# Optimization experiments

Measured on AMD Instinct MI355X. Metric: run time of the kernel, lower is better.

Reference implementation:

```python
import jax, jax.numpy as jnp
import numpy as np

INPUT_DIM = 1024
OUTPUT_DIM = 1024
DEGREE = 8


def setup_inputs() -> dict:
    key = jax.random.key(0)
    k1, k2 = jax.random.split(key)
    x = jax.random.normal(k1, (8192, INPUT_DIM), dtype=jnp.float32)
    std = 1.0 / (INPUT_DIM * (DEGREE + 1))
    cheby_coeffs = jax.random.normal(k2, (INPUT_DIM, OUTPUT_DIM, DEGREE + 1), dtype=jnp.float32) * std
    return {"x": x, "cheby_coeffs": cheby_coeffs}


def reference(x, cheby_coeffs):
    # x: [B, I]; cheby_coeffs: [I, O, D+1]
    degree = cheby_coeffs.shape[-1] - 1
    t = jnp.clip(jnp.tanh(x), -0.999, 0.999)            # [B, I]
    theta = jnp.arccos(t)[..., None]                     # [B, I, 1]
    arange = jnp.arange(degree + 1, dtype=x.dtype)       # [D+1]
    basis = jnp.cos(theta * arange)                      # [B, I, D+1] Chebyshev T_d(t)
    y = jnp.einsum('bid,iod->bo', basis, cheby_coeffs)   # [B, O]
    return y
```

## Files before the change

### kernel.cpp

```cpp
#include <hip/hip_runtime.h>
#include <stdint.h>

#define B_ROWS 8192
#define I_DIM  1024
#define N_DIM  1024
#define NDEG   9
#define K_DIM  (I_DIM * (NDEG-1))

#define BM 256
#define BN 128
#define BK 64
#define NT (K_DIM / BK)

typedef __attribute__((ext_vector_type(8)))  short short8;
typedef __attribute__((ext_vector_type(16))) float f32x16;

__device__ __forceinline__ unsigned short f2bf(float f) {
  union { float f; uint32_t u; } v; v.f = f;
  uint32_t u = v.u;
  u += 0x7FFFu + ((u >> 16) & 1u);
  return (unsigned short)(u >> 16);
}

__device__ __forceinline__ float bf2f(unsigned short h) {
  union { uint32_t u; float f; } v; v.u = ((uint32_t)h) << 16;
  return v.f;
}

__device__ __forceinline__ int h2(int r) { return (r >> 2) & 7; }

__global__ __launch_bounds__(256) void prep_kernel(const float* __restrict__ x,
                                                   const float* __restrict__ cf,
                                                   unsigned short* __restrict__ A,
                                                   unsigned short* __restrict__ Bt,
                                                   float* __restrict__ bias,
                                                   int repack_blocks) {
  __shared__ unsigned short L[32][584];
  const int tid = threadIdx.x;

  if ((int)blockIdx.x < repack_blocks) {
    const int bx = blockIdx.x;
    const int i0 = (bx & 31) * 32;
    const int o0 = (bx >> 5) * 64;

    #pragma unroll
    for (int j = 0; j < 18; ++j) {
      const int f4  = j * 256 + tid;
      const int il  = f4 / 144;
      const int odq = f4 % 144;
      const float4 v = *reinterpret_cast<const float4*>(
          cf + ((size_t)(i0 + il) * N_DIM + o0) * NDEG + (size_t)odq * 4);
      ushort4 w;
      w.x = f2bf(v.x); w.y = f2bf(v.y); w.z = f2bf(v.z); w.w = f2bf(v.w);
      *reinterpret_cast<ushort4*>(&L[il][odq * 4]) = w;
    }
    __syncthreads();

    for (int od = tid; od < 576; od += 256) {
      const int o = od / 9, d = od % 9;
      if (d == 0) {
        float s = 0.f;
        #pragma unroll
        for (int il = 0; il < 32; ++il) s += bf2f(L[il][od]);
        atomicAdd(&bias[o0 + o], s);
      } else {
        const size_t base = (size_t)(o0 + o) * K_DIM + (size_t)(d - 1) * I_DIM + i0;
        #pragma unroll
        for (int ci = 0; ci < 4; ++ci) {
          uint32_t uu[4];
          #pragma unroll
          for (int p = 0; p < 4; ++p) {
            unsigned short lo = L[ci * 8 + p * 2 + 0][od];
            unsigned short hi = L[ci * 8 + p * 2 + 1][od];
            uu[p] = (uint32_t)lo | ((uint32_t)hi << 16);
          }
          uint4 u; u.x = uu[0]; u.y = uu[1]; u.z = uu[2]; u.w = uu[3];
          *reinterpret_cast<uint4*>(Bt + base + ci * 8) = u;
        }
      }
    }
  } else {
    const int b  = blockIdx.x - repack_blocks;
    const int i0 = tid * 4;
    const float4 xv = *reinterpret_cast<const float4*>(x + (size_t)b * I_DIM + i0);
    float t[4];
    t[0] = fminf(fmaxf(tanhf(xv.x), -0.999f), 0.999f);
    t[1] = fminf(fmaxf(tanhf(xv.y), -0.999f), 0.999f);
    t[2] = fminf(fmaxf(tanhf(xv.z), -0.999f), 0.999f);
    t[3] = fminf(fmaxf(tanhf(xv.w), -0.999f), 0.999f);

    unsigned short* outb = A + (size_t)b * K_DIM + i0;
    float Tp[4] = {1.f, 1.f, 1.f, 1.f};
    float Tc[4] = {t[0], t[1], t[2], t[3]};
    #pragma unroll
    for (int d = 1; d < NDEG; ++d) {
      ushort4 o4;
      o4.x = f2bf(Tc[0]); o4.y = f2bf(Tc[1]); o4.z = f2bf(Tc[2]); o4.w = f2bf(Tc[3]);
      *reinterpret_cast<ushort4*>(outb + (size_t)(d - 1) * I_DIM) = o4;
      if (d < NDEG - 1) {
        #pragma unroll
        for (int j = 0; j < 4; ++j) {
          float Tn = 2.0f * t[j] * Tc[j] - Tp[j];
          Tp[j] = Tc[j]; Tc[j] = Tn;
        }
      }
    }
  }
}

__global__ __launch_bounds__(512, 2) void gemm_kernel(const unsigned short* __restrict__ A,
                                                      const unsigned short* __restrict__ Bt,
                                                      const float* __restrict__ bias,
                                                      float* __restrict__ C) {
  extern __shared__ unsigned short sm[];
  const int tid  = threadIdx.x;
  const int lane = tid & 63;
  const int wave = tid >> 6;
  const int l31  = lane & 31;
  const int half = lane >> 5;
  const int wm   = wave >> 1;
  const int wn   = wave & 1;
  const int m0   = blockIdx.x * BM;
  const int n0   = blockIdx.y * BN;

  const int sr   = tid >> 3;
  const int slot = tid & 7;

  const unsigned short* Abase = A  + (size_t)m0 * K_DIM;
  const unsigned short* Bbase = Bt + (size_t)n0 * K_DIM;

  f32x16 acc[2][2];
  #pragma unroll
  for (int a = 0; a < 2; ++a)
    #pragma unroll
    for (int b = 0; b < 2; ++b)
      #pragma unroll
      for (int r = 0; r < 16; ++r)
        acc[a][b][r] = 0.f;

#define STAGE_A(s, bf, kk) { const int r_ = (s)*64 + sr; const int gc_ = slot ^ h2(r_);     \
    __builtin_amdgcn_global_load_lds(                                                       \
        (const __attribute__((address_space(1))) void*)(Abase + (size_t)r_*K_DIM + (kk) + gc_*8), \
        (__attribute__((address_space(3))) void*)&sm[(bf)*16384 + r_*64 + slot*8], 16, 0, 0); }
#define STAGE_B(s, bf, kk) { const int r_ = (s)*64 + sr; const int gc_ = slot ^ h2(r_);     \
    __builtin_amdgcn_global_load_lds(                                                       \
        (const __attribute__((address_space(1))) void*)(Bbase + (size_t)r_*K_DIM + (kk) + gc_*8), \
        (__attribute__((address_space(3))) void*)&sm[32768 + (bf)*8192 + r_*64 + slot*8], 16, 0, 0); }

  STAGE_A(0, 0, 0) STAGE_A(1, 0, 0) STAGE_A(2, 0, 0) STAGE_A(3, 0, 0)
  STAGE_B(0, 0, 0) STAGE_B(1, 0, 0)

  const int rowA0 = wm * 64 + l31;
  const int rowA1 = wm * 64 + 32 + l31;
  const int rowB0 = wn * 64 + l31;
  const int rowB1 = wn * 64 + 32 + l31;

  for (int kt = 0; kt < NT; ++kt) {
    const int  cur  = kt & 1;
    const int  nxt  = cur ^ 1;
    const int  k1   = (kt + 1) * BK;
    const bool more = (kt + 1 < NT);
    const unsigned short* Asc = &sm[cur * 16384];
    const unsigned short* Bsc = &sm[32768 + cur * 8192];

    if (more) { STAGE_A(0, nxt, k1) STAGE_A(1, nxt, k1) }
    if (more) asm volatile("s_waitcnt vmcnt(2)" ::: "memory");
    else      asm volatile("s_waitcnt vmcnt(0)" ::: "memory");
    __builtin_amdgcn_s_barrier();
    __builtin_amdgcn_sched_barrier(0);

    short8 av0[4], av1[4], bv0[4], bv1[4];
    #pragma unroll
    for (int ks = 0; ks < 4; ++ks) {
      const int c = ks * 2 + half;
      av0[ks] = *reinterpret_cast<const short8*>(&Asc[rowA0 * 64 + (c ^ h2(rowA0)) * 8]);
      bv0[ks] = *reinterpret_cast<const short8*>(&Bsc[rowB0 * 64 + (c ^ h2(rowB0)) * 8]);
    }
    __builtin_amdgcn_s_setprio(1);
    #pragma unroll
    for (int ks = 0; ks < 4; ++ks)
      acc[0][0] = __builtin_amdgcn_mfma_f32_32x32x16_bf16(av0[ks], bv0[ks], acc[0][0], 0, 0, 0);
    __builtin_amdgcn_s_setprio(0);
    __builtin_amdgcn_s_barrier();

    #pragma unroll
    for (int ks = 0; ks < 4; ++ks) {
      const int c = ks * 2 + half;
      bv1[ks] = *reinterpret_cast<const short8*>(&Bsc[rowB1 * 64 + (c ^ h2(rowB1)) * 8]);
    }
    if (more) { STAGE_A(2, nxt, k1) STAGE_A(3, nxt, k1) }
    __builtin_amdgcn_s_barrier();
    __builtin_amdgcn_s_setprio(1);
    #pragma unroll
    for (int ks = 0; ks < 4; ++ks)
      acc[0][1] = __builtin_amdgcn_mfma_f32_32x32x16_bf16(av0[ks], bv1[ks], acc[0][1], 0, 0, 0);
    __builtin_amdgcn_s_setprio(0);
    __builtin_amdgcn_s_barrier();

    #pragma unroll
    for (int ks = 0; ks < 4; ++ks) {
      const int c = ks * 2 + half;
      av1[ks] = *reinterpret_cast<const short8*>(&Asc[rowA1 * 64 + (c ^ h2(rowA1)) * 8]);
    }
    if (more) { STAGE_B(0, nxt, k1) STAGE_B(1, nxt, k1) }
    __builtin_amdgcn_s_barrier();
    __builtin_amdgcn_s_setprio(1);
    #pragma unroll
    for (int ks = 0; ks < 4; ++ks) {
      acc[1][0] = __builtin_amdgcn_mfma_f32_32x32x16_bf16(av1[ks], bv0[ks], acc[1][0], 0, 0, 0);
      acc[1][1] = __builtin_amdgcn_mfma_f32_32x32x16_bf16(av1[ks], bv1[ks], acc[1][1], 0, 0, 0);
    }
    __builtin_amdgcn_s_setprio(0);
    __builtin_amdgcn_s_barrier();
    __builtin_amdgcn_sched_barrier(0);
  }
#undef STAGE_A
#undef STAGE_B

  #pragma unroll
  for (int ni = 0; ni < 2; ++ni) {
    const int col  = n0 + wn * 64 + ni * 32 + l31;
    const float bc = bias[col];
    #pragma unroll
    for (int mi = 0; mi < 2; ++mi) {
      const int rbase = m0 + wm * 64 + mi * 32 + 4 * half;
      #pragma unroll
      for (int r = 0; r < 16; ++r) {
        const int row = rbase + (r & 3) + 8 * (r >> 2);
        C[(size_t)row * N_DIM + col] = acc[mi][ni][r] + bc;
      }
    }
  }
}

extern "C" void kernel_launch(void* const* d_in, const int* in_sizes, int n_in,
                              void* d_out, int out_size, void* d_ws, size_t ws_size,
                              hipStream_t stream) {
  const float* x      = (const float*)d_in[0];
  const float* coeffs = (const float*)d_in[1];
  float* y            = (float*)d_out;

  const size_t bt_bytes = (size_t)N_DIM * K_DIM * sizeof(unsigned short);
  unsigned short* Bt = (unsigned short*)d_ws;
  float* bias        = (float*)((char*)d_ws + bt_bytes);
  unsigned short* A  = (unsigned short*)((char*)d_ws + bt_bytes + 4096);

  hipMemsetAsync(bias, 0, N_DIM * sizeof(float), stream);

  hipFuncSetAttribute((const void*)gemm_kernel,
                      hipFuncAttributeMaxDynamicSharedMemorySize, 98304);

  size_t avail    = (ws_size > bt_bytes + 4096) ? (ws_size - bt_bytes - 4096) : 0;
  size_t rows_fit = avail / ((size_t)K_DIM * sizeof(unsigned short));
  int m_chunk = (int)((rows_fit / BM) * BM);
  if (m_chunk > B_ROWS) m_chunk = B_ROWS;
  if (m_chunk < BM)     m_chunk = BM;

  for (int m0 = 0; m0 < B_ROWS; m0 += m_chunk) {
    int mc = B_ROWS - m0; if (mc > m_chunk) mc = m_chunk;
    const int rb = (m0 == 0) ? 512 : 0;
    prep_kernel<<<rb + mc, 256, 0, stream>>>(x + (size_t)m0 * I_DIM, coeffs, A, Bt, bias, rb);
    gemm_kernel<<<dim3(mc / BM, N_DIM / BN), 512, 98304, stream>>>(
        A, Bt, bias, y + (size_t)m0 * N_DIM);
  }
}
```

Baseline: 274.6 us.

## Switch GEMM main loop to triple-buffered LDS with one barrier per k-tile

The main loop moves from a double-buffered LDS scheme with four barriers per k-tile and interleaved partial staging to a three-stage ring. Tile kt+2 is prefetched while tile kt is computed, and all LDS fragments are loaded up front so the 16 MFMAs run back to back. Only one waitcnt plus barrier is needed per iteration. This raises LDS use to 144 KB per block, which should still fit one 512-thread block per CU. The cost is more VGPRs held for fragments.

```diff
diff --git a/kernel.cpp b/kernel.cpp
--- a/kernel.cpp
+++ b/kernel.cpp
@@ -145,77 +145,58 @@
 #define STAGE_B(s, bf, kk) { const int r_ = (s)*64 + sr; const int gc_ = slot ^ h2(r_);     \
     __builtin_amdgcn_global_load_lds(                                                       \
         (const __attribute__((address_space(1))) void*)(Bbase + (size_t)r_*K_DIM + (kk) + gc_*8), \
-        (__attribute__((address_space(3))) void*)&sm[32768 + (bf)*8192 + r_*64 + slot*8], 16, 0, 0); }
-
-  STAGE_A(0, 0, 0) STAGE_A(1, 0, 0) STAGE_A(2, 0, 0) STAGE_A(3, 0, 0)
-  STAGE_B(0, 0, 0) STAGE_B(1, 0, 0)
+        (__attribute__((address_space(3))) void*)&sm[49152 + (bf)*8192 + r_*64 + slot*8], 16, 0, 0); }
+#define STAGE6(bf, kk) { STAGE_A(0, bf, kk) STAGE_A(1, bf, kk) STAGE_A(2, bf, kk) STAGE_A(3, bf, kk) \
+                         STAGE_B(0, bf, kk) STAGE_B(1, bf, kk) }
+
+  STAGE6(0, 0)
+  STAGE6(1, BK)
+  asm volatile("s_waitcnt vmcnt(6)" ::: "memory");
+  __builtin_amdgcn_s_barrier();
 
   const int rowA0 = wm * 64 + l31;
   const int rowA1 = wm * 64 + 32 + l31;
   const int rowB0 = wn * 64 + l31;
   const int rowB1 = wn * 64 + 32 + l31;
 
+  int cur = 0;
   for (int kt = 0; kt < NT; ++kt) {
-    const int  cur  = kt & 1;
-    const int  nxt  = cur ^ 1;
-    const int  k1   = (kt + 1) * BK;
-    const bool more = (kt + 1 < NT);
     const unsigned short* Asc = &sm[cur * 16384];
-    const unsigned short* Bsc = &sm[32768 + cur * 8192];
-
-    if (more) { STAGE_A(0, nxt, k1) STAGE_A(1, nxt, k1) }
-    if (more) asm volatile("s_waitcnt vmcnt(2)" ::: "memory");
-    else      asm volatile("s_waitcnt vmcnt(0)" ::: "memory");
-    __builtin_amdgcn_s_barrier();
-    __builtin_amdgcn_sched_barrier(0);
-
-    short8 av0[4], av1[4], bv0[4], bv1[4];
+    const unsigned short* Bsc = &sm[49152 + cur * 8192];
+    const int s2 = (cur == 0) ? 2 : cur - 1;
+
+    short8 av[2][4], bv[2][4];
     #pragma unroll
     for (int ks = 0; ks < 4; ++ks) {
       const int c = ks * 2 + half;
-      av0[ks] = *reinterpret_cast<const short8*>(&Asc[rowA0 * 64 + (c ^ h2(rowA0)) * 8]);
-      bv0[ks] = *reinterpret_cast<const short8*>(&Bsc[rowB0 * 64 + (c ^ h2(rowB0)) * 8]);
-    }
+      av[0][ks] = *reinterpret_cast<const short8*>(&Asc[rowA0 * 64 + (c ^ h2(rowA0)) * 8]);
+      av[1][ks] = *reinterpret_cast<const short8*>(&Asc[rowA1 * 64 + (c ^ h2(rowA1)) * 8]);
+      bv[0][ks] = *reinterpret_cast<const short8*>(&Bsc[rowB0 * 64 + (c ^ h2(rowB0)) * 8]);
+      bv[1][ks] = *reinterpret_cast<const short8*>(&Bsc[rowB1 * 64 + (c ^ h2(rowB1)) * 8]);
+    }
+
+    if (kt + 2 < NT) { STAGE6(s2, (kt + 2) * BK) }
+
     __builtin_amdgcn_s_setprio(1);
     #pragma unroll
-    for (int ks = 0; ks < 4; ++ks)
-      acc[0][0] = __builtin_amdgcn_mfma_f32_32x32x16_bf16(av0[ks], bv0[ks], acc[0][0], 0, 0, 0);
+    for (int ks = 0; ks < 4; ++ks) {
+      acc[0][0] = __builtin_amdgcn_mfma_f32_32x32x16_bf16(av[0][ks], bv[0][ks], acc[0][0], 0, 0, 0);
+      acc[0][1] = __builtin_amdgcn_mfma_f32_32x32x16_bf16(av[0][ks], bv[1][ks], acc[0][1], 0, 0, 0);
+      acc[1][0] = __builtin_amdgcn_mfma_f32_32x32x16_bf16(av[1][ks], bv[0][ks], acc[1][0], 0, 0, 0);
+      acc[1][1] = __builtin_amdgcn_mfma_f32_32x32x16_bf16(av[1][ks], bv[1][ks], acc[1][1], 0, 0, 0);
+    }
     __builtin_amdgcn_s_setprio(0);
-    __builtin_amdgcn_s_barrier();
-
-    #pragma unroll
-    for (int ks = 0; ks < 4; ++ks) {
-      const int c = ks * 2 + half;
-      bv1[ks] = *reinterpret_cast<const short8*>(&Bsc[rowB1 * 64 + (c ^ h2(rowB1)) * 8]);
-    }
-    if (more) { STAGE_A(2, nxt, k1) STAGE_A(3, nxt, k1) }
-    __builtin_amdgcn_s_barrier();
-    __builtin_amdgcn_s_setprio(1);
-    #pragma unroll
-    for (int ks = 0; ks < 4; ++ks)
-      acc[0][1] = __builtin_amdgcn_mfma_f32_32x32x16_bf16(av0[ks], bv1[ks], acc[0][1], 0, 0, 0);
-    __builtin_amdgcn_s_setprio(0);
-    __builtin_amdgcn_s_barrier();
-
-    #pragma unroll
-    for (int ks = 0; ks < 4; ++ks) {
-      const int c = ks * 2 + half;
-      av1[ks] = *reinterpret_cast<const short8*>(&Asc[rowA1 * 64 + (c ^ h2(rowA1)) * 8]);
-    }
-    if (more) { STAGE_B(0, nxt, k1) STAGE_B(1, nxt, k1) }
-    __builtin_amdgcn_s_barrier();
-    __builtin_amdgcn_s_setprio(1);
-    #pragma unroll
-    for (int ks = 0; ks < 4; ++ks) {
-      acc[1][0] = __builtin_amdgcn_mfma_f32_32x32x16_bf16(av1[ks], bv0[ks], acc[1][0], 0, 0, 0);
-      acc[1][1] = __builtin_amdgcn_mfma_f32_32x32x16_bf16(av1[ks], bv1[ks], acc[1][1], 0, 0, 0);
-    }
-    __builtin_amdgcn_s_setprio(0);
-    __builtin_amdgcn_s_barrier();
-    __builtin_amdgcn_sched_barrier(0);
+
+    if (kt < NT - 1) {
+      if (kt < NT - 2) asm volatile("s_waitcnt vmcnt(6)" ::: "memory");
+      else             asm volatile("s_waitcnt vmcnt(0)" ::: "memory");
+      __builtin_amdgcn_s_barrier();
+    }
+    cur = (cur == 2) ? 0 : cur + 1;
   }
 #undef STAGE_A
 #undef STAGE_B
+#undef STAGE6
 
   #pragma unroll
   for (int ni = 0; ni < 2; ++ni) {
@@ -248,7 +229,7 @@
   hipMemsetAsync(bias, 0, N_DIM * sizeof(float), stream);
 
   hipFuncSetAttribute((const void*)gemm_kernel,
-                      hipFuncAttributeMaxDynamicSharedMemorySize, 98304);
+                      hipFuncAttributeMaxDynamicSharedMemorySize, 147456);
 
   size_t avail    = (ws_size > bt_bytes + 4096) ? (ws_size - bt_bytes - 4096) : 0;
   size_t rows_fit = avail / ((size_t)K_DIM * sizeof(unsigned short));
@@ -260,7 +241,7 @@
     int mc = B_ROWS - m0; if (mc > m_chunk) mc = m_chunk;
     const int rb = (m0 == 0) ? 512 : 0;
     prep_kernel<<<rb + mc, 256, 0, stream>>>(x + (size_t)m0 * I_DIM, coeffs, A, Bt, bias, rb);
-    gemm_kernel<<<dim3(mc / BM, N_DIM / BN), 512, 98304, stream>>>(
+    gemm_kernel<<<dim3(mc / BM, N_DIM / BN), 512, 147456, stream>>>(
         A, Bt, bias, y + (size_t)m0 * N_DIM);
   }
 }
```

Result: slower. 286.6 us (+4.4%).
